# Performance work log

Measured on AMD Instinct MI355X. Metric: run time of the kernel, lower is better.

Reference implementation:

```python
import jax, jax.numpy as jnp
import numpy as np

K = 31            # kernel_size
P = K // 2        # padding
EPS = 1e-05
STRENGTH = 1.0


def _box_filter(x):
    """31x31 mean box filter with zero padding, done as two separable 1D passes.
    Exactly equals F.conv2d(x, ones(K,K)/K^2, padding=P) since the box kernel
    is separable and padding is zero-fill."""
    kh = jnp.ones((1, 1, K, 1), x.dtype) / K  # vertical pass
    kw = jnp.ones((1, 1, 1, K), x.dtype) / K  # horizontal pass
    dn = jax.lax.conv_dimension_numbers(x.shape, kh.shape, ('NCHW', 'OIHW', 'NCHW'))
    x = jax.lax.conv_general_dilated(x, kh, (1, 1), [(P, P), (0, 0)], dimension_numbers=dn)
    x = jax.lax.conv_general_dilated(x, kw, (1, 1), [(0, 0), (P, P)], dimension_numbers=dn)
    return x


def setup_inputs() -> dict:
    key = jax.random.key(0)
    # (B, 1, H, W) image in [0, 1]
    x = jax.random.uniform(key, (32, 1, 1024, 1024), dtype=jnp.float32)
    return {"x": x}


def reference(x):
    local_mean = _box_filter(x)
    local_sq_mean = _box_filter(x * x)
    local_var = local_sq_mean - local_mean * local_mean
    local_std = jnp.sqrt(jnp.maximum(local_var, EPS))  # clamp(min=eps) then sqrt
    normalized = (x - local_mean) / (local_std + EPS)
    enhanced = jax.nn.sigmoid(normalized * 0.5)
    return x * (1.0 - STRENGTH) + enhanced * STRENGTH
```

## Files before the change

kernel.cpp:

```cpp
#include <hip/hip_runtime.h>
#include <math.h>


#define KSZ    31
#define PAD    15
#define IMG_H  1024
#define IMG_W  1024
#define SH     64
#define RPP    8
#define PHASES (SH / RPP)
#define NT     512
#define LROW   66
#define LBUF   (16 * LROW)
#define EPSV   1e-5f

#define LDS_BARRIER() do {                                   \
    asm volatile("s_waitcnt lgkmcnt(0)" ::: "memory");       \
    __builtin_amdgcn_s_barrier();                            \
} while (0)

__global__ __launch_bounds__(NT, 4)
void lcn_fused_kernel(const float* __restrict__ x, float* __restrict__ out) {
    const int cpx = gridDim.x >> 3;
    const int bid = (blockIdx.x & 7) * cpx + (blockIdx.x >> 3);

    const int chunk = bid & 15;
    const int b     = bid >> 4;
    const int y0    = chunk * SH;

    const float* img  = x   + (size_t)b * (IMG_H * IMG_W);
    float*       oimg = out + (size_t)b * (IMG_H * IMG_W);

    __shared__ float2 vbuf[RPP][LBUF];

    const int t    = threadIdx.x;
    const int wave = t >> 6;
    const int lane = t & 63;

    for (int i = t; i < RPP * 32; i += NT) {
        const int r = i >> 5, k = i & 31;
        float2* vb = vbuf[r];
        if (k < 16) vb[k * LROW] = make_float2(0.f, 0.f);
        else        vb[(k - 16) * LROW + (LROW - 1)] = make_float2(0.f, 0.f);
    }

    const int c0 = 2 * t;
    float vs0 = 0.f, vs1 = 0.f, vq0 = 0.f, vq1 = 0.f;
    for (int y = y0 - PAD; y <= y0 + PAD; ++y) {
        const int yc = max(y, 0);
        float2 v = *(const float2*)(img + (size_t)yc * IMG_W + c0);
        const float m = (y >= 0) ? 1.f : 0.f;
        v.x *= m; v.y *= m;
        vs0 += v.x; vq0 = fmaf(v.x, v.x, vq0);
        vs1 += v.y; vq1 = fmaf(v.y, v.y, vq1);
    }

    float2 sb[RPP], ad[RPP];
    #pragma unroll
    for (int r = 0; r < RPP; ++r) {
        const int ys  = y0 + r - PAD;
        const int ya  = y0 + r + PAD + 1;
        const int ysc = max(ys, 0);
        float2 vS = *(const float2*)(img + (size_t)ysc * IMG_W + c0);
        float2 vA = *(const float2*)(img + (size_t)ya  * IMG_W + c0);
        const float mS = (ys >= 0) ? 1.f : 0.f;
        sb[r] = make_float2(vS.x * mS, vS.y * mS);
        ad[r] = vA;
    }

    const int iv0 = c0 + 16;
    const int wp0 = ((iv0    ) & 15) * LROW + ((iv0    ) >> 4);
    const int wp1 = ((iv0 + 1) & 15) * LROW + ((iv0 + 1) >> 4);

    const int   cbase = lane << 4;
    const float inv   = 1.0f / 961.0f;

    for (int ph = 0; ph < PHASES; ++ph) {
        const int yo = y0 + ph * RPP;

        #pragma unroll
        for (int r = 0; r < RPP; ++r) {
            vbuf[r][wp0] = make_float2(vs0, vq0);
            vbuf[r][wp1] = make_float2(vs1, vq1);
            vs0 += ad[r].x - sb[r].x;
            vq0 = fmaf(ad[r].x, ad[r].x, vq0); vq0 = fmaf(-sb[r].x, sb[r].x, vq0);
            vs1 += ad[r].y - sb[r].y;
            vq1 = fmaf(ad[r].y, ad[r].y, vq1); vq1 = fmaf(-sb[r].y, sb[r].y, vq1);
        }
        LDS_BARRIER();

        if (ph < PHASES - 1) {
            const int yn = yo + RPP;
            if (yn >= PAD && yn <= IMG_H - RPP - PAD - 1) {
                #pragma unroll
                for (int r = 0; r < RPP; ++r) {
                    sb[r] = *(const float2*)(img + (size_t)(yn + r - PAD) * IMG_W + c0);
                    ad[r] = *(const float2*)(img + (size_t)(yn + r + PAD + 1) * IMG_W + c0);
                }
            } else {
                #pragma unroll
                for (int r = 0; r < RPP; ++r) {
                    const int ys  = yn + r - PAD;
                    const int ya  = yn + r + PAD + 1;
                    const int ysc = max(ys, 0);
                    const int yac = min(ya, IMG_H - 1);
                    float2 vS = *(const float2*)(img + (size_t)ysc * IMG_W + c0);
                    float2 vA = *(const float2*)(img + (size_t)yac * IMG_W + c0);
                    const float mS = (ys >= 0)    ? 1.f : 0.f;
                    const float mA = (ya < IMG_H) ? 1.f : 0.f;
                    sb[r] = make_float2(vS.x * mS, vS.y * mS);
                    ad[r] = make_float2(vA.x * mA, vA.y * mA);
                }
            }
        }

        {
            const int row = yo + wave;
            const float* xr = img + (size_t)row * IMG_W + cbase;
            float4 xa = ((const float4*)xr)[0];
            float4 xb = ((const float4*)xr)[1];
            float4 xc = ((const float4*)xr)[2];
            float4 xd = ((const float4*)xr)[3];

            const float2* vr = &vbuf[wave][lane];
            float hs = 0.f, hq = 0.f;
            #pragma unroll
            for (int s = 1; s <= 31; ++s) {
                float2 v = vr[(s & 15) * LROW + (s >> 4)];
                hs += v.x; hq += v.y;
            }
            float xs[16] = { xa.x, xa.y, xa.z, xa.w,  xb.x, xb.y, xb.z, xb.w,
                             xc.x, xc.y, xc.z, xc.w,  xd.x, xd.y, xd.z, xd.w };
            float res[16];
            #pragma unroll
            for (int j = 0; j < 16; ++j) {
                if (j > 0) {
                    float2 va  = vr[((j - 1) & 15) * LROW + 2];
                    float2 vsu = vr[(j & 15) * LROW];
                    hs += va.x - vsu.x;
                    hq += va.y - vsu.y;
                }
                const float mean = hs * inv;
                const float var  = fmaf(-mean, mean, hq * inv);
                const float stdv = sqrtf(fmaxf(var, EPSV));
                const float norm = (xs[j] - mean) *
                                   __builtin_amdgcn_rcpf(stdv + EPSV);
                res[j] = __builtin_amdgcn_rcpf(1.0f + __expf(-0.5f * norm));
            }
            float* orow = oimg + (size_t)row * IMG_W + cbase;
            ((float4*)orow)[0] = make_float4(res[0],  res[1],  res[2],  res[3]);
            ((float4*)orow)[1] = make_float4(res[4],  res[5],  res[6],  res[7]);
            ((float4*)orow)[2] = make_float4(res[8],  res[9],  res[10], res[11]);
            ((float4*)orow)[3] = make_float4(res[12], res[13], res[14], res[15]);
        }
        LDS_BARRIER();
    }
}

extern "C" void kernel_launch(void* const* d_in, const int* in_sizes, int n_in,
                              void* d_out, int out_size, void* d_ws, size_t ws_size,
                              hipStream_t stream) {
    (void)n_in; (void)out_size; (void)d_ws; (void)ws_size;
    const float* x = (const float*)d_in[0];
    float* out = (float*)d_out;
    const int B = in_sizes[0] / (IMG_H * IMG_W);
    dim3 grid(B * (IMG_H / SH));
    lcn_fused_kernel<<<grid, NT, 0, stream>>>(x, out);
}
```

Measured before the change: 90.25 us.

## Warp-specialize producer/consumer waves with double-buffered LDS for vertical sums

Splits the block into four producer waves, which compute vertical running sums four columns at a time and write them into a double-buffered LDS ring, and four consumer waves, which do the horizontal pass and the output math. Each phase now needs one barrier instead of two, so producer and consumer work can overlap. The horizontal initial sum is also split into two accumulators to shorten the dependency chain. The trade-off is that only half the threads do each stage, which may unbalance the work if the consumer math dominates.

```diff
diff --git a/kernel.cpp b/kernel.cpp
--- a/kernel.cpp
+++ b/kernel.cpp
@@ -7,8 +7,8 @@
 #define IMG_H  1024
 #define IMG_W  1024
 #define SH     64
-#define RPP    8
-#define PHASES (SH / RPP)
+#define GP     4
+#define NPH    (SH / GP)
 #define NT     512
 #define LROW   66
 #define LBUF   (16 * LROW)
@@ -31,104 +31,139 @@
     const float* img  = x   + (size_t)b * (IMG_H * IMG_W);
     float*       oimg = out + (size_t)b * (IMG_H * IMG_W);
 
-    __shared__ float2 vbuf[RPP][LBUF];
+    __shared__ float2 vbuf[2][GP][LBUF];
 
     const int t    = threadIdx.x;
     const int wave = t >> 6;
     const int lane = t & 63;
 
-    for (int i = t; i < RPP * 32; i += NT) {
-        const int r = i >> 5, k = i & 31;
-        float2* vb = vbuf[r];
+    if (t < 256) {
+        const int s = t >> 5;
+        const int k = t & 31;
+        float2* vb = &vbuf[s >> 2][s & 3][0];
         if (k < 16) vb[k * LROW] = make_float2(0.f, 0.f);
         else        vb[(k - 16) * LROW + (LROW - 1)] = make_float2(0.f, 0.f);
     }
 
-    const int c0 = 2 * t;
-    float vs0 = 0.f, vs1 = 0.f, vq0 = 0.f, vq1 = 0.f;
-    for (int y = y0 - PAD; y <= y0 + PAD; ++y) {
-        const int yc = max(y, 0);
-        float2 v = *(const float2*)(img + (size_t)yc * IMG_W + c0);
-        const float m = (y >= 0) ? 1.f : 0.f;
-        v.x *= m; v.y *= m;
-        vs0 += v.x; vq0 = fmaf(v.x, v.x, vq0);
-        vs1 += v.y; vq1 = fmaf(v.y, v.y, vq1);
-    }
-
-    float2 sb[RPP], ad[RPP];
-    #pragma unroll
-    for (int r = 0; r < RPP; ++r) {
-        const int ys  = y0 + r - PAD;
-        const int ya  = y0 + r + PAD + 1;
-        const int ysc = max(ys, 0);
-        float2 vS = *(const float2*)(img + (size_t)ysc * IMG_W + c0);
-        float2 vA = *(const float2*)(img + (size_t)ya  * IMG_W + c0);
-        const float mS = (ys >= 0) ? 1.f : 0.f;
-        sb[r] = make_float2(vS.x * mS, vS.y * mS);
-        ad[r] = vA;
-    }
-
-    const int iv0 = c0 + 16;
-    const int wp0 = ((iv0    ) & 15) * LROW + ((iv0    ) >> 4);
-    const int wp1 = ((iv0 + 1) & 15) * LROW + ((iv0 + 1) >> 4);
-
-    const int   cbase = lane << 4;
-    const float inv   = 1.0f / 961.0f;
-
-    for (int ph = 0; ph < PHASES; ++ph) {
-        const int yo = y0 + ph * RPP;
+    const float inv = 1.0f / 961.0f;
+
+    if (wave >= 4) {
+        const int pt = t & 255;
+        const int c0 = 4 * pt;
+
+        const int iv  = c0 + 16;
+        const int wp0 = ((iv    ) & 15) * LROW + ((iv    ) >> 4);
+        const int wp1 = ((iv + 1) & 15) * LROW + ((iv + 1) >> 4);
+        const int wp2 = ((iv + 2) & 15) * LROW + ((iv + 2) >> 4);
+        const int wp3 = ((iv + 3) & 15) * LROW + ((iv + 3) >> 4);
+
+        float vs0=0,vs1=0,vs2=0,vs3=0, vq0=0,vq1=0,vq2=0,vq3=0;
+        for (int y = y0 - PAD; y <= y0 + PAD; ++y) {
+            const int yc = max(y, 0);
+            float4 v = *(const float4*)(img + (size_t)yc * IMG_W + c0);
+            const float m = (y >= 0) ? 1.f : 0.f;
+            v.x *= m; v.y *= m; v.z *= m; v.w *= m;
+            vs0 += v.x; vq0 = fmaf(v.x, v.x, vq0);
+            vs1 += v.y; vq1 = fmaf(v.y, v.y, vq1);
+            vs2 += v.z; vq2 = fmaf(v.z, v.z, vq2);
+            vs3 += v.w; vq3 = fmaf(v.w, v.w, vq3);
+        }
 
         #pragma unroll
-        for (int r = 0; r < RPP; ++r) {
-            vbuf[r][wp0] = make_float2(vs0, vq0);
-            vbuf[r][wp1] = make_float2(vs1, vq1);
-            vs0 += ad[r].x - sb[r].x;
-            vq0 = fmaf(ad[r].x, ad[r].x, vq0); vq0 = fmaf(-sb[r].x, sb[r].x, vq0);
-            vs1 += ad[r].y - sb[r].y;
-            vq1 = fmaf(ad[r].y, ad[r].y, vq1); vq1 = fmaf(-sb[r].y, sb[r].y, vq1);
-        }
-        LDS_BARRIER();
-
-        if (ph < PHASES - 1) {
-            const int yn = yo + RPP;
-            if (yn >= PAD && yn <= IMG_H - RPP - PAD - 1) {
+        for (int r = 0; r < GP; ++r) {
+            vbuf[0][r][wp0] = make_float2(vs0, vq0);
+            vbuf[0][r][wp1] = make_float2(vs1, vq1);
+            vbuf[0][r][wp2] = make_float2(vs2, vq2);
+            vbuf[0][r][wp3] = make_float2(vs3, vq3);
+            const int ys  = y0 + r - PAD;
+            const int ya  = y0 + r + PAD + 1;
+            const int ysc = max(ys, 0);
+            float4 vS = *(const float4*)(img + (size_t)ysc * IMG_W + c0);
+            float4 vA = *(const float4*)(img + (size_t)ya  * IMG_W + c0);
+            const float mS = (ys >= 0) ? 1.f : 0.f;
+            float s0 = vS.x*mS, s1 = vS.y*mS, s2 = vS.z*mS, s3 = vS.w*mS;
+            vs0 += vA.x - s0; vq0 = fmaf(vA.x, vA.x, vq0); vq0 = fmaf(-s0, s0, vq0);
+            vs1 += vA.y - s1; vq1 = fmaf(vA.y, vA.y, vq1); vq1 = fmaf(-s1, s1, vq1);
+            vs2 += vA.z - s2; vq2 = fmaf(vA.z, vA.z, vq2); vq2 = fmaf(-s2, s2, vq2);
+            vs3 += vA.w - s3; vq3 = fmaf(vA.w, vA.w, vq3); vq3 = fmaf(-s3, s3, vq3);
+        }
+
+        float4 pfS[GP], pfA[GP];
+        {
+            const int base = y0 + GP;
+            #pragma unroll
+            for (int r = 0; r < GP; ++r) {
+                const int ys = base + r - PAD;
+                const int ya = base + r + PAD + 1;
+                pfS[r] = *(const float4*)(img + (size_t)max(ys, 0) * IMG_W + c0);
+                pfA[r] = *(const float4*)(img + (size_t)min(ya, IMG_H - 1) * IMG_W + c0);
+            }
+        }
+
+        for (int p = 0; p < NPH; ++p) {
+            LDS_BARRIER();
+            if (p < NPH - 1) {
+                const int base = y0 + GP * (p + 1);
+                float2* dst = &vbuf[(p + 1) & 1][0][0];
                 #pragma unroll
-                for (int r = 0; r < RPP; ++r) {
-                    sb[r] = *(const float2*)(img + (size_t)(yn + r - PAD) * IMG_W + c0);
-                    ad[r] = *(const float2*)(img + (size_t)(yn + r + PAD + 1) * IMG_W + c0);
-                }
-            } else {
-                #pragma unroll
-                for (int r = 0; r < RPP; ++r) {
-                    const int ys  = yn + r - PAD;
-                    const int ya  = yn + r + PAD + 1;
-                    const int ysc = max(ys, 0);
-                    const int yac = min(ya, IMG_H - 1);
-                    float2 vS = *(const float2*)(img + (size_t)ysc * IMG_W + c0);
-                    float2 vA = *(const float2*)(img + (size_t)yac * IMG_W + c0);
+                for (int r = 0; r < GP; ++r) {
+                    float2* d = dst + r * LBUF;
+                    d[wp0] = make_float2(vs0, vq0);
+                    d[wp1] = make_float2(vs1, vq1);
+                    d[wp2] = make_float2(vs2, vq2);
+                    d[wp3] = make_float2(vs3, vq3);
+                    const int ys = base + r - PAD;
+                    const int ya = base + r + PAD + 1;
                     const float mS = (ys >= 0)    ? 1.f : 0.f;
                     const float mA = (ya < IMG_H) ? 1.f : 0.f;
-                    sb[r] = make_float2(vS.x * mS, vS.y * mS);
-                    ad[r] = make_float2(vA.x * mA, vA.y * mA);
-                }
-            }
-        }
-
-        {
-            const int row = yo + wave;
+                    float s0 = pfS[r].x*mS, s1 = pfS[r].y*mS,
+                          s2 = pfS[r].z*mS, s3 = pfS[r].w*mS;
+                    float a0 = pfA[r].x*mA, a1 = pfA[r].y*mA,
+                          a2 = pfA[r].z*mA, a3 = pfA[r].w*mA;
+                    vs0 += a0 - s0; vq0 = fmaf(a0, a0, vq0); vq0 = fmaf(-s0, s0, vq0);
+                    vs1 += a1 - s1; vq1 = fmaf(a1, a1, vq1); vq1 = fmaf(-s1, s1, vq1);
+                    vs2 += a2 - s2; vq2 = fmaf(a2, a2, vq2); vq2 = fmaf(-s2, s2, vq2);
+                    vs3 += a3 - s3; vq3 = fmaf(a3, a3, vq3); vq3 = fmaf(-s3, s3, vq3);
+                }
+                if (p < NPH - 2) {
+                    const int base2 = y0 + GP * (p + 2);
+                    #pragma unroll
+                    for (int r = 0; r < GP; ++r) {
+                        const int ys = base2 + r - PAD;
+                        const int ya = base2 + r + PAD + 1;
+                        pfS[r] = *(const float4*)(img + (size_t)max(ys, 0) * IMG_W + c0);
+                        pfA[r] = *(const float4*)(img + (size_t)min(ya, IMG_H - 1) * IMG_W + c0);
+                    }
+                }
+            }
+        }
+    } else {
+        const int cbase = lane << 4;
+
+        for (int p = 0; p < NPH; ++p) {
+            LDS_BARRIER();
+            const int row = y0 + GP * p + wave;
+
             const float* xr = img + (size_t)row * IMG_W + cbase;
             float4 xa = ((const float4*)xr)[0];
             float4 xb = ((const float4*)xr)[1];
             float4 xc = ((const float4*)xr)[2];
             float4 xd = ((const float4*)xr)[3];
 
-            const float2* vr = &vbuf[wave][lane];
-            float hs = 0.f, hq = 0.f;
+            const float2* vr = &vbuf[p & 1][wave][lane];
+
+            float hsA = 0.f, hqA = 0.f, hsB = 0.f, hqB = 0.f;
             #pragma unroll
-            for (int s = 1; s <= 31; ++s) {
-                float2 v = vr[(s & 15) * LROW + (s >> 4)];
-                hs += v.x; hq += v.y;
-            }
+            for (int s = 1; s <= 31; s += 2) {
+                float2 va = vr[(s & 15) * LROW + (s >> 4)];
+                hsA += va.x; hqA += va.y;
+                if (s + 1 <= 31) {
+                    float2 vb2 = vr[((s + 1) & 15) * LROW + ((s + 1) >> 4)];
+                    hsB += vb2.x; hqB += vb2.y;
+                }
+            }
+            float hs = hsA + hsB, hq = hqA + hqB;
+
             float xs[16] = { xa.x, xa.y, xa.z, xa.w,  xb.x, xb.y, xb.z, xb.w,
                              xc.x, xc.y, xc.z, xc.w,  xd.x, xd.y, xd.z, xd.w };
             float res[16];
@@ -147,13 +182,13 @@
                                    __builtin_amdgcn_rcpf(stdv + EPSV);
                 res[j] = __builtin_amdgcn_rcpf(1.0f + __expf(-0.5f * norm));
             }
+
             float* orow = oimg + (size_t)row * IMG_W + cbase;
             ((float4*)orow)[0] = make_float4(res[0],  res[1],  res[2],  res[3]);
             ((float4*)orow)[1] = make_float4(res[4],  res[5],  res[6],  res[7]);
             ((float4*)orow)[2] = make_float4(res[8],  res[9],  res[10], res[11]);
             ((float4*)orow)[3] = make_float4(res[12], res[13], res[14], res[15]);
         }
-        LDS_BARRIER();
     }
 }
 
```

Result: faster. 85.37 us, median of 2 (-5.4%).
